# Kernel tuning notes

Measured on AMD Instinct MI355X. Metric: run time of the kernel, lower is better.

Reference implementation:

```python
import jax, jax.numpy as jnp
import numpy as np

NEG_SLOPE = 0.2
LN_EPS = 1e-5


def _layernorm(x, g, b):
    mu = jnp.mean(x, axis=-1, keepdims=True)
    var = jnp.mean(jnp.square(x - mu), axis=-1, keepdims=True)
    return (x - mu) * jax.lax.rsqrt(var + LN_EPS) * g + b


def _gat_layer(x, src, dst, ew, W, al, ar, bias, resW, act):
    # x: [N, F_in], W: [F_in, H*D], al/ar: [H, D], bias: [H*D]
    N = x.shape[0]
    H, D = al.shape
    feat = (x @ W).reshape(N, H, D)
    el = jnp.einsum('nhd,hd->nh', feat, al)          # [N, H]
    er = jnp.einsum('nhd,hd->nh', feat, ar)          # [N, H]
    e = jax.nn.leaky_relu(el[src] + er[dst], NEG_SLOPE)  # [E, H]
    # segment softmax over incoming edges of each destination node
    emax = jax.ops.segment_max(e, dst, num_segments=N)
    emax = jnp.where(jnp.isfinite(emax), emax, 0.0)
    ex = jnp.exp(e - emax[dst])
    den = jax.ops.segment_sum(ex, dst, num_segments=N)
    a = ex / den[dst] * ew[:, None]                  # [E, H] (edge_weight scales post-softmax, DGL semantics)
    msg = feat[src] * a[:, :, None]                  # [E, H, D]
    rst = jax.ops.segment_sum(msg, dst, num_segments=N)  # [N, H, D]
    res = (x @ resW).reshape(N, H, D) if resW is not None else x.reshape(N, H, D)
    rst = rst + res + bias.reshape(1, H, D)
    if act is not None:
        rst = act(rst)
    return rst.reshape(N, H * D)


def setup_inputs() -> dict:
    key = jax.random.key(0)
    ks = jax.random.split(key, 24)
    N, E, F_in, H, D = 100000, 1600000, 256, 4, 32
    HD = H * D
    s = 0.1
    inp = {
        'x': jax.random.normal(ks[0], (N, F_in), jnp.float32),
        'src': jax.random.randint(ks[1], (E,), 0, N, jnp.int32),
        'dst': jax.random.randint(ks[2], (E,), 0, N, jnp.int32),
        'edge_weight': jax.random.uniform(ks[3], (E,), jnp.float32),
        # layer 0: in 256 -> 4 heads x 32, residual Linear
        'W0': jax.random.normal(ks[4], (F_in, HD), jnp.float32) * s,
        'al0': jax.random.normal(ks[5], (H, D), jnp.float32) * s,
        'ar0': jax.random.normal(ks[6], (H, D), jnp.float32) * s,
        'b0': jnp.zeros((HD,), jnp.float32),
        'resW0': jax.random.normal(ks[7], (F_in, HD), jnp.float32) * s,
        'ln0_g': jnp.ones((HD,), jnp.float32),
        'ln0_b': jnp.zeros((HD,), jnp.float32),
        # layer 1: 128 -> 4x32, identity residual
        'W1': jax.random.normal(ks[8], (HD, HD), jnp.float32) * s,
        'al1': jax.random.normal(ks[9], (H, D), jnp.float32) * s,
        'ar1': jax.random.normal(ks[10], (H, D), jnp.float32) * s,
        'b1': jnp.zeros((HD,), jnp.float32),
        'ln1_g': jnp.ones((HD,), jnp.float32),
        'ln1_b': jnp.zeros((HD,), jnp.float32),
        # layer 2 (last, no activation)
        'W2': jax.random.normal(ks[11], (HD, HD), jnp.float32) * s,
        'al2': jax.random.normal(ks[12], (H, D), jnp.float32) * s,
        'ar2': jax.random.normal(ks[13], (H, D), jnp.float32) * s,
        'b2': jnp.zeros((HD,), jnp.float32),
        'ln2_g': jnp.ones((HD,), jnp.float32),
        'ln2_b': jnp.zeros((HD,), jnp.float32),
    }
    return inp


def reference(x, src, dst, edge_weight,
              W0, al0, ar0, b0, resW0, ln0_g, ln0_b,
              W1, al1, ar1, b1, ln1_g, ln1_b,
              W2, al2, ar2, b2, ln2_g, ln2_b):
    h = _gat_layer(x, src, dst, edge_weight, W0, al0, ar0, b0, resW0, jax.nn.elu)
    h = _layernorm(h, ln0_g, ln0_b)
    h = _gat_layer(h, src, dst, edge_weight, W1, al1, ar1, b1, None, jax.nn.elu)
    h = _layernorm(h, ln1_g, ln1_b)
    h = _gat_layer(h, src, dst, edge_weight, W2, al2, ar2, b2, None, None)
    h = _layernorm(h, ln2_g, ln2_b)
    return h
```

## Files before the change

### kernel.cpp

```cpp
#include <hip/hip_runtime.h>
#include <hip/hip_bf16.h>
#include <hip/hip_fp16.h>
#include <math.h>

#define DEV __device__ __forceinline__

typedef short v8s __attribute__((ext_vector_type(8)));
typedef float v4f __attribute__((ext_vector_type(4)));
typedef __fp16 fp16x2 __attribute__((ext_vector_type(2)));

DEV float bf2f(unsigned short u) {
    union { unsigned int i; float f; } c; c.i = ((unsigned int)u) << 16; return c.f;
}
DEV unsigned short f2bf(float f) {
    union { float f; unsigned int u; } c; c.f = f;
    unsigned int u = c.u;
    unsigned int r = u + 0x7fffu + ((u >> 16) & 1u);
    return (unsigned short)(r >> 16);
}
DEV unsigned short f2h(float f) {
    union { _Float16 h; unsigned short u; } c; c.h = (_Float16)f; return c.u;
}
DEV float h2f(unsigned short u) {
    union { unsigned short u; _Float16 h; } c; c.u = u; return (float)c.h;
}
DEV unsigned int pkdup(float x) {
    union { fp16x2 h; unsigned int u; } c;
    c.h = __builtin_amdgcn_cvt_pkrtz(x, x);
    return c.u;
}
DEV __half2 bitcast_h2(unsigned int u) {
    union { unsigned int u; __half2 h; } c; c.u = u; return c.h;
}

#if __has_builtin(__builtin_amdgcn_exp2f)
DEV float fexp2(float x) { return __builtin_amdgcn_exp2f(x); }
#else
DEV float fexp2(float x) { float r; asm("v_exp_f32 %0, %1" : "=v"(r) : "v"(x)); return r; }
#endif
#if __has_builtin(__builtin_amdgcn_rcpf)
DEV float frcp(float x) { return __builtin_amdgcn_rcpf(x); }
#else
DEV float frcp(float x) { float r; asm("v_rcp_f32 %0, %1" : "=v"(r) : "v"(x)); return r; }
#endif
#if __has_builtin(__builtin_amdgcn_rsqf)
DEV float frsq(float x) { return __builtin_amdgcn_rsqf(x); }
#else
DEV float frsq(float x) { float r; asm("v_rsq_f32 %0, %1" : "=v"(r) : "v"(x)); return r; }
#endif
DEV unsigned int cvtpk_bf16(float lo, float hi) {
    unsigned int r;
    asm("v_cvt_pk_bf16_f32 %0, %1, %2" : "=v"(r) : "v"(lo), "v"(hi));
    return r;
}

__global__ void detect_kernel(const unsigned short* __restrict__ w, int* __restrict__ flag) {
    __shared__ int cnt;
    if (threadIdx.x == 0) cnt = 0;
    __syncthreads();
    int c = 0;
    for (int i = threadIdx.x; i < 2048; i += 256) {
        unsigned short u = w[i * 2];
        int e = (u >> 7) & 0xff;
        if (e >= 110 && e <= 132) c++;
    }
    atomicAdd(&cnt, c);
    __syncthreads();
    if (threadIdx.x == 0) *flag = (cnt > 1024) ? 1 : 0;
}


__global__ void zero_kernel(int* __restrict__ p, int n) {
    int i = blockIdx.x * 256 + threadIdx.x;
    if (i < n) p[i] = 0;
}

__global__ void degree_kernel(const int* __restrict__ dst, int* __restrict__ deg, int E) {
    int i = blockIdx.x * 256 + threadIdx.x;
    if (i < E) atomicAdd(&deg[dst[i]], 1);
}

__global__ __launch_bounds__(1024)
void pscan_kernel(const int* __restrict__ deg, int* __restrict__ rowptr,
                  int* __restrict__ bsum, int n) {
    __shared__ int wtot[16];
    const int tid  = threadIdx.x;
    const int lane = tid & 63;
    const int wid  = tid >> 6;
    const int i0 = blockIdx.x * 4096 + tid * 4;
    int v0 = (i0     < n) ? deg[i0]     : 0;
    int v1 = (i0 + 1 < n) ? deg[i0 + 1] : 0;
    int v2 = (i0 + 2 < n) ? deg[i0 + 2] : 0;
    int v3 = (i0 + 3 < n) ? deg[i0 + 3] : 0;
    int s = v0 + v1 + v2 + v3;
    int sc = s;
    #pragma unroll
    for (int d = 1; d < 64; d <<= 1) {
        int t = __shfl_up(sc, d);
        if (lane >= d) sc += t;
    }
    if (lane == 63) wtot[wid] = sc;
    __syncthreads();
    int woff = 0, tot = 0;
    #pragma unroll
    for (int w = 0; w < 16; ++w) {
        int t = wtot[w];
        if (w < wid) woff += t;
        tot += t;
    }
    int p = woff + (sc - s);
    if (i0     < n) rowptr[i0]     = p; p += v0;
    if (i0 + 1 < n) rowptr[i0 + 1] = p; p += v1;
    if (i0 + 2 < n) rowptr[i0 + 2] = p; p += v2;
    if (i0 + 3 < n) rowptr[i0 + 3] = p;
    if (tid == 0) bsum[blockIdx.x] = tot;
}

__global__ void bscan_kernel(const int* __restrict__ bsum, int* __restrict__ boff, int nb) {
    int lane = threadIdx.x & 63;
    int v = (lane < nb) ? bsum[lane] : 0;
    int sc = v;
    #pragma unroll
    for (int d = 1; d < 64; d <<= 1) {
        int t = __shfl_up(sc, d);
        if (lane >= d) sc += t;
    }
    if (lane < nb) boff[lane] = sc - v;
}

__global__ void addoff_kernel(int* __restrict__ rowptr, const int* __restrict__ boff,
                              int n, int E) {
    int i = blockIdx.x * 256 + threadIdx.x;
    if (i < n) rowptr[i] += boff[i >> 12];
    else if (i == n) rowptr[n] = E;
}

__global__ void scatter_kernel(const int* __restrict__ src, const int* __restrict__ dst,
                               const void* __restrict__ ew, const int* __restrict__ flagp,
                               const int* __restrict__ rowptr, int* __restrict__ deg,
                               int2* __restrict__ csr, int E) {
    int i = blockIdx.x * 256 + threadIdx.x;
    if (i < E) {
        int isbf = *flagp;
        int d = dst[i];
        int pos = atomicAdd(&deg[d], -1) - 1;
        int slot = rowptr[d] + pos;
        float wv = isbf ? bf2f(((const unsigned short*)ew)[i]) : ((const float*)ew)[i];
        csr[slot] = make_int2(src[i], __float_as_int(wv));
    }
}

__global__ void wtrans_kernel(const void* __restrict__ B, unsigned short* __restrict__ Btp,
                              const int* __restrict__ flagp, int K) {
    int i = blockIdx.x * 256 + threadIdx.x;
    if (i >= 128 * K) return;
    int j = i & 7;
    int l = (i >> 3) & 63;
    int t = (i >> 9) & 7;
    int c = i >> 12;
    int k = c * 32 + ((l >> 4) * 8) + j;
    int n = t * 16 + (l & 15);
    unsigned short v;
    if (*flagp) v = ((const unsigned short*)B)[k * 128 + n];
    else        v = f2bf(((const float*)B)[k * 128 + n]);
    Btp[i] = v;
}

DEV void elr_epilogue(const v4f* acc, const void* al, const void* ar, int isbf,
                      int r, int quad, long m0, int M,
                      float4* el4, float4* er4) {
    float alv[8], arv[8];
    if (isbf) {
        const unsigned short* alp = (const unsigned short*)al;
        const unsigned short* arp = (const unsigned short*)ar;
        #pragma unroll
        for (int h = 0; h < 4; ++h) {
            alv[2*h]   = bf2f(alp[h*32 + r]);
            alv[2*h+1] = bf2f(alp[h*32 + 16 + r]);
            arv[2*h]   = bf2f(arp[h*32 + r]);
            arv[2*h+1] = bf2f(arp[h*32 + 16 + r]);
        }
    } else {
        const float* alp = (const float*)al;
        const float* arp = (const float*)ar;
        #pragma unroll
        for (int h = 0; h < 4; ++h) {
            alv[2*h]   = alp[h*32 + r];
            alv[2*h+1] = alp[h*32 + 16 + r];
            arv[2*h]   = arp[h*32 + r];
            arv[2*h+1] = arp[h*32 + 16 + r];
        }
    }
    #pragma unroll
    for (int reg = 0; reg < 4; ++reg) {
        float pel[4], per[4];
        #pragma unroll
        for (int h = 0; h < 4; ++h) {
            pel[h] = fmaf(acc[2*h+1][reg], alv[2*h+1], acc[2*h][reg] * alv[2*h]);
            per[h] = fmaf(acc[2*h+1][reg], arv[2*h+1], acc[2*h][reg] * arv[2*h]);
        }
        #pragma unroll
        for (int d = 1; d < 16; d <<= 1) {
            #pragma unroll
            for (int h = 0; h < 4; ++h) {
                pel[h] += __shfl_xor(pel[h], d);
                per[h] += __shfl_xor(per[h], d);
            }
        }
        long grow = m0 + quad * 4 + reg;
        if (grow < M) {
            if (r == 0) el4[grow] = make_float4(pel[0], pel[1], pel[2], pel[3]);
            if (r == 1) er4[grow] = make_float4(per[0], per[1], per[2], per[3]);
        }
    }
}

__global__ __launch_bounds__(256)
void gemm0_dual(const void* __restrict__ x, const int* __restrict__ flagp,
                const unsigned short* __restrict__ Bt,
                const unsigned short* __restrict__ Btr,
                const void* __restrict__ al, const void* __restrict__ ar,
                unsigned short* __restrict__ feat,
                unsigned short* __restrict__ res_bf,
                float4* __restrict__ el4, float4* __restrict__ er4,
                int M, int K) {
    __shared__ unsigned short ldsB[8192];
    const int isbf = *flagp;
    const int lane = threadIdx.x & 63;
    const int wid  = threadIdx.x >> 6;
    const long tile = (long)blockIdx.x * 4 + wid;
    const long m0 = tile * 16;
    const int r = lane & 15, quad = lane >> 4;
    long arow = m0 + r; if (arow >= M) arow = M - 1;
    const int woff = wid * 1024 + lane * 8;
    const int loff = lane * 8;
    const int nk = K >> 5;

    v4f accA[8], accB[8];
    #pragma unroll
    for (int t = 0; t < 8; ++t) { accA[t] = (v4f){0,0,0,0}; accB[t] = (v4f){0,0,0,0}; }

    uint4 s0, s1, s2, s3;
    float4 a0, a1;
    uint4  au;
    s0 = *(const uint4*)(Bt  + woff);
    s1 = *(const uint4*)(Bt  + woff + 512);
    s2 = *(const uint4*)(Btr + woff);
    s3 = *(const uint4*)(Btr + woff + 512);
    if (isbf) {
        au = *(const uint4*)((const unsigned short*)x + (size_t)arow * K + quad * 8);
    } else {
        const float* ap = (const float*)x + (size_t)arow * K + quad * 8;
        a0 = *(const float4*)ap; a1 = *(const float4*)(ap + 4);
    }

    for (int k = 0; k < nk; ++k) {
        __syncthreads();
        *(uint4*)&ldsB[woff]              = s0;
        *(uint4*)&ldsB[woff + 512]        = s1;
        *(uint4*)&ldsB[4096 + woff]       = s2;
        *(uint4*)&ldsB[4096 + woff + 512] = s3;
        __syncthreads();
        v8s af;
        if (isbf) {
            union { uint4 u; v8s v; } c; c.u = au; af = c.v;
        } else {
            union { uint4 u; v8s v; } c;
            c.u = make_uint4(cvtpk_bf16(a0.x, a0.y), cvtpk_bf16(a0.z, a0.w),
                             cvtpk_bf16(a1.x, a1.y), cvtpk_bf16(a1.z, a1.w));
            af = c.v;
        }
        if (k + 1 < nk) {
            const unsigned short* bb = Bt  + (size_t)(k + 1) * 4096 + woff;
            const unsigned short* br = Btr + (size_t)(k + 1) * 4096 + woff;
            s0 = *(const uint4*)bb; s1 = *(const uint4*)(bb + 512);
            s2 = *(const uint4*)br; s3 = *(const uint4*)(br + 512);
            if (isbf) {
                au = *(const uint4*)((const unsigned short*)x + (size_t)arow * K + (k + 1) * 32 + quad * 8);
            } else {
                const float* ap = (const float*)x + (size_t)arow * K + (k + 1) * 32 + quad * 8;
                a0 = *(const float4*)ap; a1 = *(const float4*)(ap + 4);
            }
        }
        #pragma unroll
        for (int t = 0; t < 8; ++t) {
            v8s bfA = *(const v8s*)&ldsB[t * 512 + loff];
            v8s bfB = *(const v8s*)&ldsB[4096 + t * 512 + loff];
            accA[t] = __builtin_amdgcn_mfma_f32_16x16x32_bf16(af, bfA, accA[t], 0, 0, 0);
            accB[t] = __builtin_amdgcn_mfma_f32_16x16x32_bf16(af, bfB, accB[t], 0, 0, 0);
        }
    }
    #pragma unroll
    for (int t = 0; t < 8; ++t) {
        const int col = t * 16 + r;
        #pragma unroll
        for (int reg = 0; reg < 4; ++reg) {
            long grow = m0 + quad * 4 + reg;
            if (grow < M) feat[grow * 128 + col] = f2h(accA[t][reg]);
        }
    }
    #pragma unroll
    for (int t = 0; t < 8; t += 2) {
        const int col0 = t * 16 + r, col1 = (t + 1) * 16 + r;
        #pragma unroll
        for (int reg = 0; reg < 4; ++reg) {
            long grow = m0 + quad * 4 + reg;
            unsigned int pk = cvtpk_bf16(accB[t][reg], accB[t + 1][reg]);
            if (grow < M) {
                res_bf[grow * 128 + col0] = (unsigned short)pk;
                res_bf[grow * 128 + col1] = (unsigned short)(pk >> 16);
            }
        }
    }
    elr_epilogue(accA, al, ar, isbf, r, quad, m0, M, el4, er4);
}

__global__ __launch_bounds__(256)
void gemm_mfma(const unsigned short* __restrict__ A,
               const unsigned short* __restrict__ Btp,
               const void* __restrict__ al, const void* __restrict__ ar,
               const int* __restrict__ flagp,
               unsigned short* __restrict__ Cout,
               float4* __restrict__ el4, float4* __restrict__ er4,
               int M, int K) {
    __shared__ unsigned short ldsB[4096];
    const int lane = threadIdx.x & 63;
    const int wid  = threadIdx.x >> 6;
    const long tile = (long)blockIdx.x * 4 + wid;
    const long m0 = tile * 16;
    const int r = lane & 15, quad = lane >> 4;
    long arow = m0 + r; if (arow >= M) arow = M - 1;
    const int woff = wid * 1024 + lane * 8;
    const int loff = lane * 8;
    const int nk = K >> 5;

    v4f acc[8];
    #pragma unroll
    for (int t = 0; t < 8; ++t) acc[t] = (v4f){0.f, 0.f, 0.f, 0.f};

    uint4 s0, s1, au;
    s0 = *(const uint4*)(Btp + woff);
    s1 = *(const uint4*)(Btp + woff + 512);
    au = *(const uint4*)(A + (size_t)arow * K + quad * 8);

    for (int k = 0; k < nk; ++k) {
        __syncthreads();
        *(uint4*)&ldsB[woff]       = s0;
        *(uint4*)&ldsB[woff + 512] = s1;
        __syncthreads();
        union { uint4 u; v8s v; } c; c.u = au;
        v8s af = c.v;
        if (k + 1 < nk) {
            const unsigned short* bb = Btp + (size_t)(k + 1) * 4096 + woff;
            s0 = *(const uint4*)bb; s1 = *(const uint4*)(bb + 512);
            au = *(const uint4*)(A + (size_t)arow * K + (k + 1) * 32 + quad * 8);
        }
        #pragma unroll
        for (int t = 0; t < 8; ++t) {
            v8s bf = *(const v8s*)&ldsB[t * 512 + loff];
            acc[t] = __builtin_amdgcn_mfma_f32_16x16x32_bf16(af, bf, acc[t], 0, 0, 0);
        }
    }
    #pragma unroll
    for (int t = 0; t < 8; ++t) {
        const int col = t * 16 + r;
        #pragma unroll
        for (int reg = 0; reg < 4; ++reg) {
            long grow = m0 + quad * 4 + reg;
            if (grow < M) Cout[grow * 128 + col] = f2h(acc[t][reg]);
        }
    }
    elr_epilogue(acc, al, ar, *flagp, r, quad, m0, M, el4, er4);
}

__global__ __launch_bounds__(256)
void aggregate_kernel(const unsigned short* __restrict__ feath,
                      const float4* __restrict__ el4,
                      const float4* __restrict__ er4,
                      const unsigned short* __restrict__ res_bf,
                      const void* __restrict__ bias,
                      const void* __restrict__ lng,
                      const void* __restrict__ lnb,
                      const int* __restrict__ flagp,
                      const int* __restrict__ rowptr,
                      const int2* __restrict__ csr,
                      unsigned short* __restrict__ out_bf,
                      float* __restrict__ out_f32,
                      int N, int apply_elu, int final_mode) {
    __shared__ unsigned int s_pw[4][256];
    const int lane = threadIdx.x & 63;
    const int wid  = threadIdx.x >> 6;
    const int v = blockIdx.x * 4 + wid;
    if (v >= N) return;
    const int isbf = *flagp;
    const int eg = lane >> 4;
    const int fl = lane & 15;
    const int hd = fl >> 2;
    const int fb = fl * 8;
    const int p0 = rowptr[v], p1 = rowptr[v + 1];
    const float4 erv = er4[v];

    float den0 = 0.f, den1 = 0.f, den2 = 0.f, den3 = 0.f;
    __half2 acch[4];
    acch[0] = acch[1] = acch[2] = acch[3] = __float2half2_rn(0.f);

    for (int eb = p0; eb < p1; eb += 64) {
        const int cnt = min(64, p1 - eb);
        int s = 0; float w = 0.f;
        if (lane < cnt) {
            int2 sw = csr[eb + lane];
            s = sw.x;
            w = __int_as_float(sw.y);
        }
        int se0 = __shfl(s, eg);
        int se1 = __shfl(s, 4 + eg);
        uint4 u0 = *(const uint4*)(feath + (size_t)se0 * 128 + fb);
        uint4 u1 = *(const uint4*)(feath + (size_t)se1 * 128 + fb);
        unsigned int pw0 = 0, pw1 = 0, pw2 = 0, pw3 = 0;
        if (lane < cnt) {
            float4 elv = el4[s];
            float t, q;
            t = elv.x + erv.x; t = fmaxf(t, 0.2f * t);
            q = fexp2(fmaf(t, 1.44269504f, -6.0f)); den0 += q; pw0 = pkdup(q * w);
            t = elv.y + erv.y; t = fmaxf(t, 0.2f * t);
            q = fexp2(fmaf(t, 1.44269504f, -6.0f)); den1 += q; pw1 = pkdup(q * w);
            t = elv.z + erv.z; t = fmaxf(t, 0.2f * t);
            q = fexp2(fmaf(t, 1.44269504f, -6.0f)); den2 += q; pw2 = pkdup(q * w);
            t = elv.w + erv.w; t = fmaxf(t, 0.2f * t);
            q = fexp2(fmaf(t, 1.44269504f, -6.0f)); den3 += q; pw3 = pkdup(q * w);
        }
        *(uint4*)&s_pw[wid][lane * 4] = make_uint4(pw0, pw1, pw2, pw3);
        const int cntr = (cnt + 7) & ~7;
        for (int e = 0; e < cntr; e += 8) {
            __half2 ae0 = bitcast_h2(s_pw[wid][(e + eg) * 4 + hd]);
            __half2 ae1 = bitcast_h2(s_pw[wid][(e + 4 + eg) * 4 + hd]);
            uint4 c0 = u0, c1 = u1;
            if (e + 8 < cntr) {
                int sn0 = __shfl(s, e + 8 + eg);
                int sn1 = __shfl(s, e + 12 + eg);
                u0 = *(const uint4*)(feath + (size_t)sn0 * 128 + fb);
                u1 = *(const uint4*)(feath + (size_t)sn1 * 128 + fb);
            }
            acch[0] = __hfma2(ae0, bitcast_h2(c0.x), acch[0]);
            acch[1] = __hfma2(ae0, bitcast_h2(c0.y), acch[1]);
            acch[2] = __hfma2(ae0, bitcast_h2(c0.z), acch[2]);
            acch[3] = __hfma2(ae0, bitcast_h2(c0.w), acch[3]);
            acch[0] = __hfma2(ae1, bitcast_h2(c1.x), acch[0]);
            acch[1] = __hfma2(ae1, bitcast_h2(c1.y), acch[1]);
            acch[2] = __hfma2(ae1, bitcast_h2(c1.z), acch[2]);
            acch[3] = __hfma2(ae1, bitcast_h2(c1.w), acch[3]);
        }
    }
    #pragma unroll
    for (int j = 0; j < 4; ++j) {
        union { __half2 h; int i; } a;
        union { int i; __half2 h; } b;
        a.h = acch[j]; b.i = __shfl_xor(a.i, 16); acch[j] = __hadd2(acch[j], b.h);
        a.h = acch[j]; b.i = __shfl_xor(a.i, 32); acch[j] = __hadd2(acch[j], b.h);
    }
    #pragma unroll
    for (int d = 1; d < 64; d <<= 1) {
        den0 += __shfl_xor(den0, d);
        den1 += __shfl_xor(den1, d);
        den2 += __shfl_xor(den2, d);
        den3 += __shfl_xor(den3, d);
    }
    float den = (hd == 0) ? den0 : (hd == 1) ? den1 : (hd == 2) ? den2 : den3;
    float invd = (p1 > p0) ? frcp(den) : 0.f;
    float acc[8];
    #pragma unroll
    for (int j = 0; j < 4; ++j) {
        acc[j * 2]     = __low2float(acch[j]);
        acc[j * 2 + 1] = __high2float(acch[j]);
    }
    uint4 ru = *(const uint4*)(res_bf + (size_t)v * 128 + fb);
    float rv[8];
    rv[0] = bf2f((unsigned short)(ru.x & 0xffffu)); rv[1] = bf2f((unsigned short)(ru.x >> 16));
    rv[2] = bf2f((unsigned short)(ru.y & 0xffffu)); rv[3] = bf2f((unsigned short)(ru.y >> 16));
    rv[4] = bf2f((unsigned short)(ru.z & 0xffffu)); rv[5] = bf2f((unsigned short)(ru.z >> 16));
    rv[6] = bf2f((unsigned short)(ru.w & 0xffffu)); rv[7] = bf2f((unsigned short)(ru.w >> 16));
    float bsv[8], gv[8], lbv[8];
    if (isbf) {
        const unsigned short* bsp = (const unsigned short*)bias + fb;
        const unsigned short* gp  = (const unsigned short*)lng + fb;
        const unsigned short* bp  = (const unsigned short*)lnb + fb;
        #pragma unroll
        for (int j = 0; j < 8; ++j) { bsv[j] = bf2f(bsp[j]); gv[j] = bf2f(gp[j]); lbv[j] = bf2f(bp[j]); }
    } else {
        const float* bsp = (const float*)bias + fb;
        const float* gp  = (const float*)lng + fb;
        const float* bp  = (const float*)lnb + fb;
        #pragma unroll
        for (int j = 0; j < 8; ++j) { bsv[j] = bsp[j]; gv[j] = gp[j]; lbv[j] = bp[j]; }
    }
    float o[8];
    float ssum = 0.f;
    #pragma unroll
    for (int j = 0; j < 8; ++j) {
        float t = acc[j] * invd + rv[j] + bsv[j];
        if (apply_elu) t = (t > 0.f) ? t : fexp2(t * 1.44269504f) - 1.0f;
        o[j] = t;
        ssum += t;
    }
    #pragma unroll
    for (int d = 1; d < 16; d <<= 1) ssum += __shfl_xor(ssum, d);
    float mu = ssum * (1.0f / 128.0f);
    float vsum = 0.f;
    #pragma unroll
    for (int j = 0; j < 8; ++j) { float dd = o[j] - mu; vsum += dd * dd; }
    #pragma unroll
    for (int d = 1; d < 16; d <<= 1) vsum += __shfl_xor(vsum, d);
    float rs = frsq(vsum * (1.0f / 128.0f) + 1e-5f);
    if (eg == 0) {
        if (final_mode && !isbf) {
            float* op = out_f32 + (size_t)v * 128 + fb;
            #pragma unroll
            for (int j = 0; j < 8; ++j) op[j] = (o[j] - mu) * rs * gv[j] + lbv[j];
        } else {
            unsigned int w[4];
            #pragma unroll
            for (int j = 0; j < 4; ++j) {
                float lo = (o[j*2]   - mu) * rs * gv[j*2]   + lbv[j*2];
                float hi = (o[j*2+1] - mu) * rs * gv[j*2+1] + lbv[j*2+1];
                w[j] = cvtpk_bf16(lo, hi);
            }
            *(uint4*)(out_bf + (size_t)v * 128 + fb) = make_uint4(w[0], w[1], w[2], w[3]);
        }
    }
}


extern "C" void kernel_launch(void* const* d_in, const int* in_sizes, int n_in,
                              void* d_out, int out_size, void* d_ws, size_t ws_size,
                              hipStream_t stream) {
    const void* x    = d_in[0];
    const int* src   = (const int*)d_in[1];
    const int* dst   = (const int*)d_in[2];
    const void* ew   = d_in[3];
    const void* W0   = d_in[4];
    const void* al0  = d_in[5];
    const void* ar0  = d_in[6];
    const void* b0   = d_in[7];
    const void* resW0= d_in[8];
    const void* ln0g = d_in[9];
    const void* ln0b = d_in[10];
    const void* W1   = d_in[11];
    const void* al1  = d_in[12];
    const void* ar1  = d_in[13];
    const void* b1   = d_in[14];
    const void* ln1g = d_in[15];
    const void* ln1b = d_in[16];
    const void* W2   = d_in[17];
    const void* al2  = d_in[18];
    const void* ar2  = d_in[19];
    const void* b2   = d_in[20];
    const void* ln2g = d_in[21];
    const void* ln2b = d_in[22];

    const int HD  = 128;
    const int Fin = in_sizes[4] / HD;
    const int N   = in_sizes[0] / Fin;
    const int E   = in_sizes[1];

    char* ws = (char*)d_ws;
    size_t off = 0;
    auto alloc = [&](size_t bytes) -> void* {
        void* p = ws + off;
        off = (off + bytes + 255) & ~(size_t)255;
        return p;
    };
    int*   flag    = (int*)alloc(256);
    unsigned short* feat  = (unsigned short*)alloc((size_t)N * 128 * 2);
    unsigned short* h_bf  = (unsigned short*)alloc((size_t)N * 128 * 2);
    unsigned short* res0  = (unsigned short*)alloc((size_t)N * 128 * 2);
    float* el      = (float*)alloc((size_t)N * 4 * 4);
    float* er      = (float*)alloc((size_t)N * 4 * 4);
    int*   rowptr  = (int*)alloc((size_t)(N + 1) * 4);
    int*   deg     = (int*)alloc((size_t)N * 4);
    int*   bsum    = (int*)alloc(256);
    int*   boff    = (int*)alloc(256);
    int2*  csr     = (int2*)alloc((size_t)E * 8);
    unsigned short* Bt0  = (unsigned short*)alloc((size_t)128 * Fin * 2);
    unsigned short* Btr0 = (unsigned short*)alloc((size_t)128 * Fin * 2);
    unsigned short* Bt1  = (unsigned short*)alloc((size_t)128 * HD * 2);
    unsigned short* Bt2  = (unsigned short*)alloc((size_t)128 * HD * 2);

    const int zb = (N + 255) / 256;
    const int eb = (E + 255) / 256;
    const int gblocks = (N + 63) / 64;
    const int ablocks = (N + 3) / 4;
    const int nb = (N + 4095) / 4096;
    const int aob = (N + 1 + 255) / 256;
    const int wtb0 = (128 * Fin + 255) / 256;
    const int wtb1 = (128 * HD + 255) / 256;

    detect_kernel<<<1, 256, 0, stream>>>((const unsigned short*)W0, flag);

    zero_kernel<<<zb, 256, 0, stream>>>(deg, N);
    degree_kernel<<<eb, 256, 0, stream>>>(dst, deg, E);
    pscan_kernel<<<nb, 1024, 0, stream>>>(deg, rowptr, bsum, N);
    bscan_kernel<<<1, 64, 0, stream>>>(bsum, boff, nb);
    addoff_kernel<<<aob, 256, 0, stream>>>(rowptr, boff, N, E);
    scatter_kernel<<<eb, 256, 0, stream>>>(src, dst, ew, flag, rowptr, deg, csr, E);

    wtrans_kernel<<<wtb0, 256, 0, stream>>>(W0,    Bt0,  flag, Fin);
    wtrans_kernel<<<wtb0, 256, 0, stream>>>(resW0, Btr0, flag, Fin);
    wtrans_kernel<<<wtb1, 256, 0, stream>>>(W1,    Bt1,  flag, HD);
    wtrans_kernel<<<wtb1, 256, 0, stream>>>(W2,    Bt2,  flag, HD);

    gemm0_dual<<<gblocks, 256, 0, stream>>>(x, flag, Bt0, Btr0, al0, ar0,
        feat, res0, (float4*)el, (float4*)er, N, Fin);
    aggregate_kernel<<<ablocks, 256, 0, stream>>>(feat, (const float4*)el, (const float4*)er,
        res0, b0, ln0g, ln0b, flag, rowptr, csr, h_bf, nullptr, N, 1, 0);

    gemm_mfma<<<gblocks, 256, 0, stream>>>(h_bf, Bt1, al1, ar1, flag, feat,
        (float4*)el, (float4*)er, N, HD);
    aggregate_kernel<<<ablocks, 256, 0, stream>>>(feat, (const float4*)el, (const float4*)er,
        h_bf, b1, ln1g, ln1b, flag, rowptr, csr, h_bf, nullptr, N, 1, 0);

    gemm_mfma<<<gblocks, 256, 0, stream>>>(h_bf, Bt2, al2, ar2, flag, feat,
        (float4*)el, (float4*)er, N, HD);
    aggregate_kernel<<<ablocks, 256, 0, stream>>>(feat, (const float4*)el, (const float4*)er,
        h_bf, b2, ln2g, ln2b, flag, rowptr, csr, (unsigned short*)d_out, (float*)d_out, N, 0, 1);
}
```

Baseline: 673.7 us.

## Fuse weight transposes with degree count and CSR scatter with the first GEMM

The four weight-transpose launches are merged with the degree-count kernel into one `prep_kernel` that assigns roles by block range. The CSR scatter kernel is folded into the layer-0 dual GEMM launch, with GEMM blocks interleaved every `s` blocks so the compute-bound GEMM tiles and the memory- and atomic-bound scatter blocks can run side by side. This removes several launches and kernel-boundary gaps. The cost is that scatter blocks now carry the GEMM kernel's LDS allocation and register footprint, which may lower their occupancy, and the block-index mapping becomes more intricate.

```diff
diff --git a/kernel.cpp b/kernel.cpp
--- a/kernel.cpp
+++ b/kernel.cpp
@@ -75,8 +75,39 @@
     if (i < n) p[i] = 0;
 }
 
-__global__ void degree_kernel(const int* __restrict__ dst, int* __restrict__ deg, int E) {
-    int i = blockIdx.x * 256 + threadIdx.x;
+DEV void wtrans_body(const void* B, unsigned short* Btp, const int* flagp, int K, int blk) {
+    int i = blk * 256 + threadIdx.x;
+    if (i >= 128 * K) return;
+    int j = i & 7;
+    int l = (i >> 3) & 63;
+    int t = (i >> 9) & 7;
+    int c = i >> 12;
+    int k = c * 32 + ((l >> 4) * 8) + j;
+    int n = t * 16 + (l & 15);
+    unsigned short v;
+    if (*flagp) v = ((const unsigned short*)B)[k * 128 + n];
+    else        v = f2bf(((const float*)B)[k * 128 + n]);
+    Btp[i] = v;
+}
+
+__global__ __launch_bounds__(256)
+void prep_kernel(const void* __restrict__ W0, const void* __restrict__ rW0,
+                 const void* __restrict__ W1, const void* __restrict__ W2,
+                 unsigned short* __restrict__ Bt0, unsigned short* __restrict__ Btr0,
+                 unsigned short* __restrict__ Bt1, unsigned short* __restrict__ Bt2,
+                 const int* __restrict__ flagp,
+                 const int* __restrict__ dst, int* __restrict__ deg,
+                 int Fin, int HD, int E, int wtb0, int wtb1) {
+    int b = blockIdx.x;
+    if (b < wtb0)        { wtrans_body(W0,  Bt0,  flagp, Fin, b); return; }
+    b -= wtb0;
+    if (b < wtb0)        { wtrans_body(rW0, Btr0, flagp, Fin, b); return; }
+    b -= wtb0;
+    if (b < wtb1)        { wtrans_body(W1,  Bt1,  flagp, HD, b); return; }
+    b -= wtb1;
+    if (b < wtb1)        { wtrans_body(W2,  Bt2,  flagp, HD, b); return; }
+    b -= wtb1;
+    int i = b * 256 + threadIdx.x;
     if (i < E) atomicAdd(&deg[dst[i]], 1);
 }
 
@@ -135,37 +166,6 @@
     else if (i == n) rowptr[n] = E;
 }
 
-__global__ void scatter_kernel(const int* __restrict__ src, const int* __restrict__ dst,
-                               const void* __restrict__ ew, const int* __restrict__ flagp,
-                               const int* __restrict__ rowptr, int* __restrict__ deg,
-                               int2* __restrict__ csr, int E) {
-    int i = blockIdx.x * 256 + threadIdx.x;
-    if (i < E) {
-        int isbf = *flagp;
-        int d = dst[i];
-        int pos = atomicAdd(&deg[d], -1) - 1;
-        int slot = rowptr[d] + pos;
-        float wv = isbf ? bf2f(((const unsigned short*)ew)[i]) : ((const float*)ew)[i];
-        csr[slot] = make_int2(src[i], __float_as_int(wv));
-    }
-}
-
-__global__ void wtrans_kernel(const void* __restrict__ B, unsigned short* __restrict__ Btp,
-                              const int* __restrict__ flagp, int K) {
-    int i = blockIdx.x * 256 + threadIdx.x;
-    if (i >= 128 * K) return;
-    int j = i & 7;
-    int l = (i >> 3) & 63;
-    int t = (i >> 9) & 7;
-    int c = i >> 12;
-    int k = c * 32 + ((l >> 4) * 8) + j;
-    int n = t * 16 + (l & 15);
-    unsigned short v;
-    if (*flagp) v = ((const unsigned short*)B)[k * 128 + n];
-    else        v = f2bf(((const float*)B)[k * 128 + n]);
-    Btp[i] = v;
-}
-
 DEV void elr_epilogue(const v4f* acc, const void* al, const void* ar, int isbf,
                       int r, int quad, long m0, int M,
                       float4* el4, float4* er4) {
@@ -216,19 +216,39 @@
 }
 
 __global__ __launch_bounds__(256)
-void gemm0_dual(const void* __restrict__ x, const int* __restrict__ flagp,
-                const unsigned short* __restrict__ Bt,
-                const unsigned short* __restrict__ Btr,
-                const void* __restrict__ al, const void* __restrict__ ar,
-                unsigned short* __restrict__ feat,
-                unsigned short* __restrict__ res_bf,
-                float4* __restrict__ el4, float4* __restrict__ er4,
-                int M, int K) {
+void gemm0_scatter(const void* __restrict__ x, const int* __restrict__ flagp,
+                   const unsigned short* __restrict__ Bt,
+                   const unsigned short* __restrict__ Btr,
+                   const void* __restrict__ al, const void* __restrict__ ar,
+                   unsigned short* __restrict__ feat,
+                   unsigned short* __restrict__ res_bf,
+                   float4* __restrict__ el4, float4* __restrict__ er4,
+                   int M, int K,
+                   const int* __restrict__ src, const int* __restrict__ dst,
+                   const void* __restrict__ ew,
+                   const int* __restrict__ rowptr, int* __restrict__ deg,
+                   int2* __restrict__ csr, int E,
+                   int gblocks, int s) {
     __shared__ unsigned short ldsB[8192];
+    const int bid = blockIdx.x;
+    const int q = bid / s, rr = bid - q * s;
+    if (!(rr == 0 && q < gblocks)) {
+        int gcount = (bid + s - 1) / s; if (gcount > gblocks) gcount = gblocks;
+        int i = (bid - gcount) * 256 + threadIdx.x;
+        if (i < E) {
+            int isbf = *flagp;
+            int d = dst[i];
+            int pos = atomicAdd(&deg[d], -1) - 1;
+            int slot = rowptr[d] + pos;
+            float wv = isbf ? bf2f(((const unsigned short*)ew)[i]) : ((const float*)ew)[i];
+            csr[slot] = make_int2(src[i], __float_as_int(wv));
+        }
+        return;
+    }
     const int isbf = *flagp;
     const int lane = threadIdx.x & 63;
     const int wid  = threadIdx.x >> 6;
-    const long tile = (long)blockIdx.x * 4 + wid;
+    const long tile = (long)q * 4 + wid;
     const long m0 = tile * 16;
     const int r = lane & 15, quad = lane >> 4;
     long arow = m0 + r; if (arow >= M) arow = M - 1;
@@ -597,19 +617,19 @@
     detect_kernel<<<1, 256, 0, stream>>>((const unsigned short*)W0, flag);
 
     zero_kernel<<<zb, 256, 0, stream>>>(deg, N);
-    degree_kernel<<<eb, 256, 0, stream>>>(dst, deg, E);
+    prep_kernel<<<2 * wtb0 + 2 * wtb1 + eb, 256, 0, stream>>>(
+        W0, resW0, W1, W2, Bt0, Btr0, Bt1, Bt2, flag, dst, deg, Fin, HD, E, wtb0, wtb1);
     pscan_kernel<<<nb, 1024, 0, stream>>>(deg, rowptr, bsum, N);
     bscan_kernel<<<1, 64, 0, stream>>>(bsum, boff, nb);
     addoff_kernel<<<aob, 256, 0, stream>>>(rowptr, boff, N, E);
-    scatter_kernel<<<eb, 256, 0, stream>>>(src, dst, ew, flag, rowptr, deg, csr, E);
-
-    wtrans_kernel<<<wtb0, 256, 0, stream>>>(W0,    Bt0,  flag, Fin);
-    wtrans_kernel<<<wtb0, 256, 0, stream>>>(resW0, Btr0, flag, Fin);
-    wtrans_kernel<<<wtb1, 256, 0, stream>>>(W1,    Bt1,  flag, HD);
-    wtrans_kernel<<<wtb1, 256, 0, stream>>>(W2,    Bt2,  flag, HD);
-
-    gemm0_dual<<<gblocks, 256, 0, stream>>>(x, flag, Bt0, Btr0, al0, ar0,
-        feat, res0, (float4*)el, (float4*)er, N, Fin);
+
+    {
+        const int total = gblocks + eb;
+        int s = total / gblocks; if (s < 1) s = 1;
+        gemm0_scatter<<<total, 256, 0, stream>>>(x, flag, Bt0, Btr0, al0, ar0,
+            feat, res0, (float4*)el, (float4*)er, N, Fin,
+            src, dst, ew, rowptr, deg, csr, E, gblocks, s);
+    }
     aggregate_kernel<<<ablocks, 256, 0, stream>>>(feat, (const float4*)el, (const float4*)er,
         res0, b0, ln0g, ln0b, flag, rowptr, csr, h_bf, nullptr, N, 1, 0);
 
```

After: 734.6 us. 1.09x slower.
